# Performance work log

Measured on AMD Instinct MI355X. Metric: run time of the kernel, lower is better.

Reference implementation:

```python
import jax, jax.numpy as jnp
import numpy as np

N, E, L, H, C, F_IN = 50000, 800000, 3, 8, 16, 128  # nodes, edges, layers, heads, per-head dim, input dim
NEG_SLOPE = 0.2


def setup_inputs() -> dict:
    key = jax.random.key(0)
    k = jax.random.split(key, 8)
    scale = 0.1
    x = jax.random.normal(k[0], (N, F_IN), dtype=jnp.float32)
    Ws = jax.random.normal(k[1], (L, F_IN, H * C), dtype=jnp.float32) * scale
    att_src = jax.random.normal(k[2], (L, H, C), dtype=jnp.float32) * scale
    att_dst = jax.random.normal(k[3], (L, H, C), dtype=jnp.float32) * scale
    biases = jnp.zeros((L, H * C), dtype=jnp.float32)
    fc_w = jax.random.normal(k[4], (H * C, C), dtype=jnp.float32) * scale
    fc_b = jnp.zeros((C,), dtype=jnp.float32)
    edge_index = jax.random.randint(k[5], (2, E), 0, N, dtype=jnp.int64)
    return {"x": x, "Ws": Ws, "att_src": att_src, "att_dst": att_dst,
            "biases": biases, "fc_w": fc_w, "fc_b": fc_b, "edge_index": edge_index}


def _gat_layer(x, W, a_src, a_dst, b, src, dst):
    # x: [N, F]; W: [F, H*C]; a_src/a_dst: [H, C]; src/dst: [E+N] (self-loops included)
    n = x.shape[0]
    h = (x @ W).reshape(n, H, C)                      # [N, H, C]
    e_src = jnp.einsum('nhc,hc->nh', h, a_src)        # [N, H]
    e_dst = jnp.einsum('nhc,hc->nh', h, a_dst)
    e = jax.nn.leaky_relu(e_src[src] + e_dst[dst], NEG_SLOPE)   # [E+N, H]
    # segment softmax over incoming edges of each target node
    emax = jax.ops.segment_max(e, dst, num_segments=n)          # [N, H]
    ex = jnp.exp(e - emax[dst])
    denom = jax.ops.segment_sum(ex, dst, num_segments=n)        # [N, H]
    alpha = ex / (denom[dst] + 1e-16)                            # [E+N, H]
    out = jax.ops.segment_sum(alpha[:, :, None] * h[src], dst, num_segments=n)  # [N, H, C]
    return out.reshape(n, H * C) + b


def reference(x, Ws, att_src, att_dst, biases, fc_w, fc_b, edge_index):
    loop = jnp.arange(N, dtype=edge_index.dtype)
    src = jnp.concatenate([edge_index[0], loop])  # add self-loops (PyG default)
    dst = jnp.concatenate([edge_index[1], loop])
    h = x
    for l in range(L):
        h = _gat_layer(h, Ws[l], att_src[l], att_dst[l], biases[l], src, dst)
        h = jax.nn.elu(h)
    return h @ fc_w + fc_b  # [N, C]
```

## Files before the change

kernel.cpp:

```cpp
#include <hip/hip_runtime.h>
#include <hip/hip_bf16.h>


#define GAT_F 128
#define GAT_H 8
#define GAT_C 16

__device__ __forceinline__ float bf2f(unsigned short u) {
    union { unsigned int i; float f; } x; x.i = ((unsigned int)u) << 16; return x.f;
}
__device__ __forceinline__ float bfhi2f(unsigned int u) {
    union { unsigned int i; float f; } x; x.i = u & 0xFFFF0000u; return x.f;
}
__device__ __forceinline__ float bflo2f(unsigned int u) {
    union { unsigned int i; float f; } x; x.i = u << 16; return x.f;
}
__device__ __forceinline__ unsigned int pk_bf16(float a, float b) {
    union { float f; unsigned int i; } ua, ub;
    ua.f = a; ub.f = b;
    unsigned int ra = (ua.i + 0x7FFFu + ((ua.i >> 16) & 1u)) >> 16;
    unsigned int rb = (ub.i + 0x7FFFu + ((ub.i >> 16) & 1u)) & 0xFFFF0000u;
    return ra | rb;
}
__device__ __forceinline__ float ldf(const void* p, size_t i, int isf32) {
    return isf32 ? ((const float*)p)[i] : bf2f(((const unsigned short*)p)[i]);
}
__device__ __forceinline__ int ldei(const int* ei, int i, int is64) {
    return is64 ? ei[2 * (size_t)i] : ei[i];
}

__global__ void k_detect(const unsigned short* __restrict__ xb,
                         const int* __restrict__ ei, int* flags) {
    __shared__ int nan_cnt, zero_cnt;
    if (threadIdx.x == 0) { nan_cnt = 0; zero_cnt = 0; }
    __syncthreads();
    int t = threadIdx.x;
    int ln = 0;
    for (int i = t; i < 8192; i += 256) {
        unsigned short u = xb[i];
        if ((u & 0x7F80) == 0x7F80) ln++;
    }
    int lz = 0;
    for (int i = t; i < 2048; i += 256) {
        if (ei[2 * i + 1] == 0) lz++;
    }
    if (ln) atomicAdd(&nan_cnt, ln);
    if (lz) atomicAdd(&zero_cnt, lz);
    __syncthreads();
    if (t == 0) {
        flags[0] = (nan_cnt > 3) ? 1 : 0;
        flags[1] = (zero_cnt > 1024) ? 1 : 0;
    }
}

__global__ void k_init_deg(int* deg, int n) {
    int i = blockIdx.x * 256 + threadIdx.x;
    if (i < n) deg[i] = 1;
}

__global__ void k_count_deg(const int* __restrict__ ei, int* deg, int E,
                            const int* __restrict__ flags) {
    int k = blockIdx.x * 256 + threadIdx.x;
    int is64 = flags[1];
    if (k < E) atomicAdd(&deg[ldei(ei, E + k, is64)], 1);
}

__global__ __launch_bounds__(256) void k_scan_blk(
    const int* __restrict__ deg, int* __restrict__ rp_local,
    int* __restrict__ bsum, int n)
{
    int b = blockIdx.x, t = threadIdx.x;
    int i0 = b * 1024 + t * 4;
    int v0 = 0, v1 = 0, v2 = 0, v3 = 0;
    if (i0 + 3 < n) {
        int4 d = *(const int4*)(deg + i0);
        v0 = d.x; v1 = d.y; v2 = d.z; v3 = d.w;
    } else {
        if (i0     < n) v0 = deg[i0];
        if (i0 + 1 < n) v1 = deg[i0 + 1];
        if (i0 + 2 < n) v2 = deg[i0 + 2];
        if (i0 + 3 < n) v3 = deg[i0 + 3];
    }
    int s = v0 + v1 + v2 + v3;
    int lane = t & 63, wid = t >> 6;
    int sc = s;
    #pragma unroll
    for (int off = 1; off < 64; off <<= 1) {
        int o = __shfl_up(sc, off);
        if (lane >= off) sc += o;
    }
    __shared__ int wsum[4];
    if (lane == 63) wsum[wid] = sc;
    __syncthreads();
    int woff = 0;
    #pragma unroll
    for (int w2 = 0; w2 < 4; w2++) if (w2 < wid) woff += wsum[w2];
    int excl = woff + sc - s;
    if (i0     < n) rp_local[i0]     = excl;
    if (i0 + 1 < n) rp_local[i0 + 1] = excl + v0;
    if (i0 + 2 < n) rp_local[i0 + 2] = excl + v0 + v1;
    if (i0 + 3 < n) rp_local[i0 + 3] = excl + v0 + v1 + v2;
    if (t == 255) bsum[b] = woff + sc;
}

__global__ __launch_bounds__(256) void k_scan_top(
    int* __restrict__ bsum, int* __restrict__ rowptr, int nb, int n)
{
    __shared__ int sh[1024];
    int t = threadIdx.x;
    for (int i = t; i < 1024; i += 256) sh[i] = (i < nb) ? bsum[i] : 0;
    __syncthreads();
    for (int off = 1; off < 1024; off <<= 1) {
        int vals[4];
        #pragma unroll
        for (int k = 0; k < 4; k++) {
            int i = t + 256 * k;
            vals[k] = (i >= off) ? sh[i - off] : 0;
        }
        __syncthreads();
        #pragma unroll
        for (int k = 0; k < 4; k++) sh[t + 256 * k] += vals[k];
        __syncthreads();
    }
    for (int i = t; i < nb; i += 256) bsum[i] = (i == 0) ? 0 : sh[i - 1];
    if (t == 0) rowptr[n] = sh[nb - 1];
}

__global__ void k_place_add(int* __restrict__ rowptr, const int* __restrict__ bsum,
                            int* __restrict__ adj, int* __restrict__ cursor, int n)
{
    int i = blockIdx.x * 256 + threadIdx.x;
    if (i < n) {
        int r = rowptr[i] + bsum[i >> 10];
        rowptr[i] = r;
        adj[r] = i;
        cursor[i] = 1;
    }
    if (blockIdx.x == 0 && threadIdx.x < 8) adj[rowptr[n] + threadIdx.x] = 0;
}

__global__ void k_scatter(const int* __restrict__ ei, const int* __restrict__ rowptr,
                          int* __restrict__ cursor, int* __restrict__ adj, int E,
                          const int* __restrict__ flags) {
    int k = blockIdx.x * 256 + threadIdx.x;
    int is64 = flags[1];
    if (k < E) {
        int s = ldei(ei, k, is64);
        int d = ldei(ei, E + k, is64);
        int p = atomicAdd(&cursor[d], 1);
        adj[rowptr[d] + p] = s;
    }
}

__global__ __launch_bounds__(256) void k_gemm_scores(
    const void* __restrict__ xin, int x_is_input,
    const void* __restrict__ W, long w_off,
    const void* __restrict__ asrc, const void* __restrict__ adst, long a_off,
    unsigned int* __restrict__ hout, float* __restrict__ es, float* __restrict__ ed,
    int n, const int* __restrict__ flags)
{
    __shared__ float xs[32 * 132];
    int isf32 = flags[0];
    int t = threadIdx.x;
    int row0 = blockIdx.x * 32;

    if (!x_is_input) {
        const float4* xg = (const float4*)xin;
        for (int i = t; i < 32 * GAT_F / 4; i += 256) {
            int r = i >> 5, k4 = i & 31;
            int gr = row0 + r;
            float4 v = make_float4(0.f, 0.f, 0.f, 0.f);
            if (gr < n) v = xg[gr * 32 + k4];
            *(float4*)&xs[r * 132 + k4 * 4] = v;
        }
    } else {
        for (int i = t; i < 32 * GAT_F; i += 256) {
            int r = i >> 7, k = i & 127;
            int gr = row0 + r;
            float v = 0.f;
            if (gr < n) v = ldf(xin, (size_t)gr * GAT_F + k, isf32);
            xs[r * 132 + k] = v;
        }
    }
    __syncthreads();

    int tx = t & 31, ty = t >> 5;
    int r0 = ty * 4, c0 = tx * 4;
    float acc[4][4];
    #pragma unroll
    for (int i = 0; i < 4; i++)
        #pragma unroll
        for (int j = 0; j < 4; j++) acc[i][j] = 0.f;

    if (isf32) {
        const float4* Wg = (const float4*)((const float*)W + w_off);
        for (int k = 0; k < GAT_F; k++) {
            float4 wv = Wg[k * 32 + tx];
            #pragma unroll
            for (int i = 0; i < 4; i++) {
                float xv = xs[(r0 + i) * 132 + k];
                acc[i][0] += xv * wv.x; acc[i][1] += xv * wv.y;
                acc[i][2] += xv * wv.z; acc[i][3] += xv * wv.w;
            }
        }
    } else {
        const ushort4* Wg = (const ushort4*)((const unsigned short*)W + w_off);
        for (int k = 0; k < GAT_F; k++) {
            ushort4 u4 = Wg[k * 32 + tx];
            float4 wv = make_float4(bf2f(u4.x), bf2f(u4.y), bf2f(u4.z), bf2f(u4.w));
            #pragma unroll
            for (int i = 0; i < 4; i++) {
                float xv = xs[(r0 + i) * 132 + k];
                acc[i][0] += xv * wv.x; acc[i][1] += xv * wv.y;
                acc[i][2] += xv * wv.z; acc[i][3] += xv * wv.w;
            }
        }
    }

    int head = tx >> 2;
    int cb = (tx & 3) * 4;
    float av[4], dv[4];
    #pragma unroll
    for (int j = 0; j < 4; j++) {
        av[j] = ldf(asrc, a_off + head * GAT_C + cb + j, isf32);
        dv[j] = ldf(adst, a_off + head * GAT_C + cb + j, isf32);
    }
    #pragma unroll
    for (int i = 0; i < 4; i++) {
        float ps = acc[i][0] * av[0] + acc[i][1] * av[1] + acc[i][2] * av[2] + acc[i][3] * av[3];
        float pd = acc[i][0] * dv[0] + acc[i][1] * dv[1] + acc[i][2] * dv[2] + acc[i][3] * dv[3];
        ps += __shfl_xor(ps, 1); ps += __shfl_xor(ps, 2);
        pd += __shfl_xor(pd, 1); pd += __shfl_xor(pd, 2);
        int gr = row0 + r0 + i;
        if ((tx & 3) == 0 && gr < n) {
            es[(size_t)gr * GAT_H + head] = ps;
            ed[(size_t)gr * GAT_H + head] = pd;
        }
        if (gr < n) {
            uint2 packed = make_uint2(pk_bf16(acc[i][0], acc[i][1]),
                                      pk_bf16(acc[i][2], acc[i][3]));
            *(uint2*)(hout + gr * 64 + (c0 >> 1)) = packed;
        }
    }
}

__global__ __launch_bounds__(256) void k_aggregate(
    const unsigned int* __restrict__ hb,
    const float* __restrict__ es, const float* __restrict__ ed,
    const int* __restrict__ rowptr, const int* __restrict__ adj,
    const void* __restrict__ bias, long b_off, float* __restrict__ out, int n,
    const int* __restrict__ flags)
{
    int isf32 = flags[0];
    int lane = threadIdx.x & 63;
    int node = blockIdx.x * 4 + (threadIdx.x >> 6);
    if (node >= n) return;
    int base = rowptr[node];
    int deg = rowptr[node + 1] - base;
    int head = lane >> 3;
    float edv = ed[node * 8 + head];

    float acc0 = 0.f, acc1 = 0.f, lsum = 0.f;
    for (int j0 = 0; j0 < deg; j0 += 4) {
        int sa = adj[base + j0];
        int sb = adj[base + j0 + 1];
        int sc = adj[base + j0 + 2];
        int sd = adj[base + j0 + 3];
        float va = es[sa * 8 + head] + edv;
        float vb = es[sb * 8 + head] + edv;
        float vc = es[sc * 8 + head] + edv;
        float vd = es[sd * 8 + head] + edv;
        unsigned int ha = hb[sa * 64 + lane];
        unsigned int hbv = hb[sb * 64 + lane];
        unsigned int hc = hb[sc * 64 + lane];
        unsigned int hd = hb[sd * 64 + lane];
        va = va > 0.f ? va : 0.2f * va;
        vb = vb > 0.f ? vb : 0.2f * vb;
        vc = vc > 0.f ? vc : 0.2f * vc;
        vd = vd > 0.f ? vd : 0.2f * vd;
        float pa = __expf(va);
        float pb = (j0 + 1 < deg) ? __expf(vb) : 0.f;
        float pc = (j0 + 2 < deg) ? __expf(vc) : 0.f;
        float pd = (j0 + 3 < deg) ? __expf(vd) : 0.f;
        lsum += (pa + pb) + (pc + pd);
        acc0 += pa * bflo2f(ha) + pb * bflo2f(hbv) + pc * bflo2f(hc) + pd * bflo2f(hd);
        acc1 += pa * bfhi2f(ha) + pb * bfhi2f(hbv) + pc * bfhi2f(hc) + pd * bfhi2f(hd);
    }

    float inv = 1.f / (lsum + 1e-16f);
    int ch = lane << 1;
    float o0 = acc0 * inv + ldf(bias, b_off + ch, isf32);
    float o1 = acc1 * inv + ldf(bias, b_off + ch + 1, isf32);
    o0 = o0 > 0.f ? o0 : (__expf(o0) - 1.f);
    o1 = o1 > 0.f ? o1 : (__expf(o1) - 1.f);
    *(float2*)(out + (size_t)node * GAT_F + ch) = make_float2(o0, o1);
}

__global__ __launch_bounds__(256) void k_fc(
    const float* __restrict__ h, const void* __restrict__ fw,
    const void* __restrict__ fb, void* __restrict__ out, int n,
    const int* __restrict__ flags)
{
    __shared__ float fws[GAT_F * GAT_C];
    int isf32 = flags[0];
    int t = threadIdx.x;
    for (int i = t; i < GAT_F * GAT_C; i += 256)
        fws[i] = ldf(fw, i, isf32);
    __syncthreads();
    int row = blockIdx.x * 256 + t;
    if (row >= n) return;
    float acc[16];
    #pragma unroll
    for (int c = 0; c < 16; c++) acc[c] = ldf(fb, c, isf32);
    const float4* hr = (const float4*)(h + (size_t)row * GAT_F);
    for (int k4 = 0; k4 < GAT_F / 4; k4++) {
        float4 xv = hr[k4];
        float xs4[4] = {xv.x, xv.y, xv.z, xv.w};
        #pragma unroll
        for (int kk = 0; kk < 4; kk++) {
            int k = k4 * 4 + kk;
            const float4* wr = (const float4*)(fws + k * GAT_C);
            #pragma unroll
            for (int c4 = 0; c4 < 4; c4++) {
                float4 wv = wr[c4];
                acc[c4 * 4 + 0] += xs4[kk] * wv.x;
                acc[c4 * 4 + 1] += xs4[kk] * wv.y;
                acc[c4 * 4 + 2] += xs4[kk] * wv.z;
                acc[c4 * 4 + 3] += xs4[kk] * wv.w;
            }
        }
    }
    if (isf32) {
        float* o = (float*)out + (size_t)row * GAT_C;
        #pragma unroll
        for (int c = 0; c < 16; c++) o[c] = acc[c];
    } else {
        __hip_bfloat16* o = (__hip_bfloat16*)out + (size_t)row * GAT_C;
        #pragma unroll
        for (int c = 0; c < 16; c++) o[c] = __float2bfloat16(acc[c]);
    }
}

extern "C" void kernel_launch(void* const* d_in, const int* in_sizes, int n_in,
                              void* d_out, int out_size, void* d_ws, size_t ws_size,
                              hipStream_t stream) {
    const void* x      = d_in[0];
    const void* Ws     = d_in[1];
    const void* att_s  = d_in[2];
    const void* att_d  = d_in[3];
    const void* biases = d_in[4];
    const void* fc_w   = d_in[5];
    const void* fc_b   = d_in[6];
    const int*  ei     = (const int*)d_in[7];

    const int N  = in_sizes[0] / GAT_F;
    const int E  = in_sizes[7] / 2;
    const int L  = in_sizes[1] / (GAT_F * GAT_F);
    const int ET = E + N;

    char* w = (char*)d_ws;
    int* flags        = (int*)w;          w += 64;
    float* hA         = (float*)w;        w += (size_t)N * GAT_F * 4;
    unsigned int* hB  = (unsigned int*)w; w += (size_t)N * 64 * 4;
    float* es         = (float*)w;        w += (size_t)N * GAT_H * 4;
    float* ed         = (float*)w;        w += (size_t)N * GAT_H * 4;
    int* rowptr       = (int*)w;          w += (((size_t)(N + 1) * 4 + 15) & ~15ull);
    int* cursor       = (int*)w;          w += (size_t)N * 4;
    int* bsum         = (int*)w;          w += 1024 * 4;
    int* adj          = (int*)w;          w += (size_t)(ET + 16) * 4;

    int nb_n = (N + 255) / 256;
    int nb_e = (E + 255) / 256;
    int nb_s = (N + 1023) / 1024;

    k_detect<<<1, 256, 0, stream>>>((const unsigned short*)x, ei, flags);

    k_init_deg<<<nb_n, 256, 0, stream>>>(cursor, N);
    k_count_deg<<<nb_e, 256, 0, stream>>>(ei, cursor, E, flags);
    k_scan_blk<<<nb_s, 256, 0, stream>>>(cursor, rowptr, bsum, N);
    k_scan_top<<<1, 256, 0, stream>>>(bsum, rowptr, nb_s, N);
    k_place_add<<<nb_n, 256, 0, stream>>>(rowptr, bsum, adj, cursor, N);
    k_scatter<<<nb_e, 256, 0, stream>>>(ei, rowptr, cursor, adj, E, flags);

    int nb_g = (N + 31) / 32;
    int nb_a = (N + 3) / 4;
    for (int l = 0; l < L; l++) {
        k_gemm_scores<<<nb_g, 256, 0, stream>>>(
            (l == 0) ? x : (const void*)hA, (l == 0) ? 1 : 0,
            Ws, (long)l * GAT_F * GAT_F,
            att_s, att_d, (long)l * GAT_H * GAT_C,
            hB, es, ed, N, flags);
        k_aggregate<<<nb_a, 256, 0, stream>>>(
            hB, es, ed, rowptr, adj,
            biases, (long)l * GAT_F, hA, N, flags);
    }
    k_fc<<<nb_n, 256, 0, stream>>>(hA, fc_w, fc_b, d_out, N, flags);
}
```

Before: 459.3 us.

## Use bf16 MFMA for layer GEMM and fold attention vectors into weights

Replaces the fp32 FMA tiled GEMM with a bf16 MFMA kernel over 64-row tiles. A prep kernel transposes the weights to bf16 and precomputes W·a_src and W·a_dst as 16 extra output columns, so the attention scores come straight out of the MFMA instead of needing shuffle reductions. This cuts GEMM compute time but adds a prep launch and rounds the inputs and score weights to bf16, which may change accuracy. It also loads the full 144x128 weight tile into shared memory in every block.

```diff
diff --git a/kernel.cpp b/kernel.cpp
--- a/kernel.cpp
+++ b/kernel.cpp
@@ -5,6 +5,9 @@
 #define GAT_F 128
 #define GAT_H 8
 #define GAT_C 16
+
+typedef __attribute__((ext_vector_type(8))) short bf16x8;
+typedef __attribute__((ext_vector_type(4))) float f32x4;
 
 __device__ __forceinline__ float bf2f(unsigned short u) {
     union { unsigned int i; float f; } x; x.i = ((unsigned int)u) << 16; return x.f;
@@ -22,6 +25,10 @@
     unsigned int rb = (ub.i + 0x7FFFu + ((ub.i >> 16) & 1u)) & 0xFFFF0000u;
     return ra | rb;
 }
+__device__ __forceinline__ unsigned short f2bf(float a) {
+    union { float f; unsigned int i; } ua; ua.f = a;
+    return (unsigned short)((ua.i + 0x7FFFu + ((ua.i >> 16) & 1u)) >> 16);
+}
 __device__ __forceinline__ float ldf(const void* p, size_t i, int isf32) {
     return isf32 ? ((const float*)p)[i] : bf2f(((const unsigned short*)p)[i]);
 }
@@ -50,6 +57,35 @@
     if (t == 0) {
         flags[0] = (nan_cnt > 3) ? 1 : 0;
         flags[1] = (zero_cnt > 1024) ? 1 : 0;
+    }
+}
+
+__global__ void k_prep(const void* __restrict__ W, const void* __restrict__ asrc,
+                       const void* __restrict__ adst,
+                       unsigned short* __restrict__ wt, unsigned short* __restrict__ wa,
+                       int Lw, const int* __restrict__ flags) {
+    int isf32 = flags[0];
+    int b = blockIdx.x, t = threadIdx.x;
+    if (b < Lw * 64) {
+        int gid = b * 256 + t;
+        int l = gid >> 14, r = gid & 16383;
+        int c = r >> 7, k = r & 127;
+        float v = ldf(W, (size_t)l * 16384 + k * 128 + c, isf32);
+        wt[gid] = f2bf(v);
+    } else {
+        int id = (b - Lw * 64) * 256 + t;
+        int l = id >> 11, q = id & 2047;
+        int j = q >> 7, k = q & 127;
+        int head = j & 7;
+        const void* av = (j < 8) ? asrc : adst;
+        float acc = 0.f;
+        #pragma unroll
+        for (int cc = 0; cc < 16; cc++) {
+            float w = ldf(W, (size_t)l * 16384 + k * 128 + head * 16 + cc, isf32);
+            float a = ldf(av, (size_t)l * 128 + head * 16 + cc, isf32);
+            acc += w * a;
+        }
+        wa[id] = f2bf(acc);
     }
 }
 
@@ -152,94 +188,89 @@
     }
 }
 
-__global__ __launch_bounds__(256) void k_gemm_scores(
+__global__ __launch_bounds__(256) void k_gemm_mfma(
     const void* __restrict__ xin, int x_is_input,
-    const void* __restrict__ W, long w_off,
-    const void* __restrict__ asrc, const void* __restrict__ adst, long a_off,
-    unsigned int* __restrict__ hout, float* __restrict__ es, float* __restrict__ ed,
+    const unsigned short* __restrict__ wt,
+    const unsigned short* __restrict__ wa,
+    unsigned int* __restrict__ hb, float* __restrict__ es, float* __restrict__ ed,
     int n, const int* __restrict__ flags)
 {
-    __shared__ float xs[32 * 132];
+    __shared__ unsigned short xl[64 * 136];
+    __shared__ unsigned short wl[144 * 136];
     int isf32 = flags[0];
     int t = threadIdx.x;
-    int row0 = blockIdx.x * 32;
-
-    if (!x_is_input) {
+    int row0 = blockIdx.x * 64;
+
+    if (isf32 || !x_is_input) {
         const float4* xg = (const float4*)xin;
-        for (int i = t; i < 32 * GAT_F / 4; i += 256) {
-            int r = i >> 5, k4 = i & 31;
+        for (int i = t; i < 2048; i += 256) {
+            int r = i >> 5, c4 = i & 31;
             int gr = row0 + r;
-            float4 v = make_float4(0.f, 0.f, 0.f, 0.f);
-            if (gr < n) v = xg[gr * 32 + k4];
-            *(float4*)&xs[r * 132 + k4 * 4] = v;
+            uint2 u = make_uint2(0u, 0u);
+            if (gr < n) {
+                float4 v = xg[(size_t)gr * 32 + c4];
+                u = make_uint2(pk_bf16(v.x, v.y), pk_bf16(v.z, v.w));
+            }
+            *(uint2*)&xl[r * 136 + c4 * 4] = u;
         }
     } else {
-        for (int i = t; i < 32 * GAT_F; i += 256) {
-            int r = i >> 7, k = i & 127;
+        const ushort4* xg = (const ushort4*)xin;
+        for (int i = t; i < 2048; i += 256) {
+            int r = i >> 5, c4 = i & 31;
             int gr = row0 + r;
-            float v = 0.f;
-            if (gr < n) v = ldf(xin, (size_t)gr * GAT_F + k, isf32);
-            xs[r * 132 + k] = v;
-        }
-    }
-    __syncthreads();
-
-    int tx = t & 31, ty = t >> 5;
-    int r0 = ty * 4, c0 = tx * 4;
-    float acc[4][4];
-    #pragma unroll
-    for (int i = 0; i < 4; i++)
-        #pragma unroll
-        for (int j = 0; j < 4; j++) acc[i][j] = 0.f;
-
-    if (isf32) {
-        const float4* Wg = (const float4*)((const float*)W + w_off);
-        for (int k = 0; k < GAT_F; k++) {
-            float4 wv = Wg[k * 32 + tx];
-            #pragma unroll
-            for (int i = 0; i < 4; i++) {
-                float xv = xs[(r0 + i) * 132 + k];
-                acc[i][0] += xv * wv.x; acc[i][1] += xv * wv.y;
-                acc[i][2] += xv * wv.z; acc[i][3] += xv * wv.w;
-            }
-        }
-    } else {
-        const ushort4* Wg = (const ushort4*)((const unsigned short*)W + w_off);
-        for (int k = 0; k < GAT_F; k++) {
-            ushort4 u4 = Wg[k * 32 + tx];
-            float4 wv = make_float4(bf2f(u4.x), bf2f(u4.y), bf2f(u4.z), bf2f(u4.w));
-            #pragma unroll
-            for (int i = 0; i < 4; i++) {
-                float xv = xs[(r0 + i) * 132 + k];
-                acc[i][0] += xv * wv.x; acc[i][1] += xv * wv.y;
-                acc[i][2] += xv * wv.z; acc[i][3] += xv * wv.w;
-            }
-        }
-    }
-
-    int head = tx >> 2;
-    int cb = (tx & 3) * 4;
-    float av[4], dv[4];
-    #pragma unroll
-    for (int j = 0; j < 4; j++) {
-        av[j] = ldf(asrc, a_off + head * GAT_C + cb + j, isf32);
-        dv[j] = ldf(adst, a_off + head * GAT_C + cb + j, isf32);
-    }
-    #pragma unroll
-    for (int i = 0; i < 4; i++) {
-        float ps = acc[i][0] * av[0] + acc[i][1] * av[1] + acc[i][2] * av[2] + acc[i][3] * av[3];
-        float pd = acc[i][0] * dv[0] + acc[i][1] * dv[1] + acc[i][2] * dv[2] + acc[i][3] * dv[3];
-        ps += __shfl_xor(ps, 1); ps += __shfl_xor(ps, 2);
-        pd += __shfl_xor(pd, 1); pd += __shfl_xor(pd, 2);
-        int gr = row0 + r0 + i;
-        if ((tx & 3) == 0 && gr < n) {
-            es[(size_t)gr * GAT_H + head] = ps;
-            ed[(size_t)gr * GAT_H + head] = pd;
-        }
-        if (gr < n) {
-            uint2 packed = make_uint2(pk_bf16(acc[i][0], acc[i][1]),
-                                      pk_bf16(acc[i][2], acc[i][3]));
-            *(uint2*)(hout + gr * 64 + (c0 >> 1)) = packed;
+            ushort4 v = make_ushort4(0, 0, 0, 0);
+            if (gr < n) v = xg[(size_t)gr * 32 + c4];
+            *(ushort4*)&xl[r * 136 + c4 * 4] = v;
+        }
+    }
+    {
+        const ushort4* wg = (const ushort4*)wt;
+        for (int i = t; i < 4096; i += 256) {
+            int c = i >> 5, k4 = i & 31;
+            *(ushort4*)&wl[c * 136 + k4 * 4] = wg[i];
+        }
+        const ushort4* wag = (const ushort4*)wa;
+        for (int i = t; i < 512; i += 256) {
+            int j = i >> 5, k4 = i & 31;
+            *(ushort4*)&wl[(128 + j) * 136 + k4 * 4] = wag[i];
+        }
+    }
+    __syncthreads();
+
+    int lane = t & 63, wid = t >> 6, quad = lane >> 4, col = lane & 15;
+    f32x4 acc[9];
+    #pragma unroll
+    for (int ct = 0; ct < 9; ct++) acc[ct] = (f32x4){0.f, 0.f, 0.f, 0.f};
+
+    #pragma unroll
+    for (int ks = 0; ks < 4; ks++) {
+        int k0 = ks * 32;
+        bf16x8 af = *(const bf16x8*)&xl[(wid * 16 + col) * 136 + k0 + quad * 8];
+        #pragma unroll
+        for (int ct = 0; ct < 9; ct++) {
+            bf16x8 bf = *(const bf16x8*)&wl[(ct * 16 + col) * 136 + k0 + quad * 8];
+            acc[ct] = __builtin_amdgcn_mfma_f32_16x16x32_bf16(af, bf, acc[ct], 0, 0, 0);
+        }
+    }
+
+    #pragma unroll
+    for (int ct = 0; ct < 8; ct++) {
+        #pragma unroll
+        for (int r = 0; r < 4; r++) {
+            int grow = row0 + wid * 16 + quad * 4 + r;
+            float v = acc[ct][r];
+            float vp = __shfl_xor(v, 1);
+            if (!(lane & 1) && grow < n)
+                hb[(size_t)grow * 64 + ct * 8 + (col >> 1)] = pk_bf16(v, vp);
+        }
+    }
+    #pragma unroll
+    for (int r = 0; r < 4; r++) {
+        int grow = row0 + wid * 16 + quad * 4 + r;
+        float v = acc[8][r];
+        if (grow < n) {
+            if (col < 8) es[(size_t)grow * 8 + col] = v;
+            else         ed[(size_t)grow * 8 + col - 8] = v;
         }
     }
 }
@@ -359,21 +390,24 @@
     const int ET = E + N;
 
     char* w = (char*)d_ws;
-    int* flags        = (int*)w;          w += 64;
-    float* hA         = (float*)w;        w += (size_t)N * GAT_F * 4;
-    unsigned int* hB  = (unsigned int*)w; w += (size_t)N * 64 * 4;
-    float* es         = (float*)w;        w += (size_t)N * GAT_H * 4;
-    float* ed         = (float*)w;        w += (size_t)N * GAT_H * 4;
-    int* rowptr       = (int*)w;          w += (((size_t)(N + 1) * 4 + 15) & ~15ull);
-    int* cursor       = (int*)w;          w += (size_t)N * 4;
-    int* bsum         = (int*)w;          w += 1024 * 4;
-    int* adj          = (int*)w;          w += (size_t)(ET + 16) * 4;
+    int* flags         = (int*)w;            w += 64;
+    float* hA          = (float*)w;          w += (size_t)N * GAT_F * 4;
+    unsigned int* hB   = (unsigned int*)w;   w += (size_t)N * 64 * 4;
+    float* es          = (float*)w;          w += (size_t)N * GAT_H * 4;
+    float* ed          = (float*)w;          w += (size_t)N * GAT_H * 4;
+    int* rowptr        = (int*)w;            w += (((size_t)(N + 1) * 4 + 15) & ~15ull);
+    int* cursor        = (int*)w;            w += (size_t)N * 4;
+    int* bsum          = (int*)w;            w += 1024 * 4;
+    int* adj           = (int*)w;            w += (size_t)(ET + 16) * 4;
+    unsigned short* wt = (unsigned short*)w; w += (size_t)L * 16384 * 2;
+    unsigned short* wa = (unsigned short*)w; w += (size_t)L * 2048 * 2;
 
     int nb_n = (N + 255) / 256;
     int nb_e = (E + 255) / 256;
     int nb_s = (N + 1023) / 1024;
 
     k_detect<<<1, 256, 0, stream>>>((const unsigned short*)x, ei, flags);
+    k_prep<<<L * 64 + L * 8, 256, 0, stream>>>(Ws, att_s, att_d, wt, wa, L, flags);
 
     k_init_deg<<<nb_n, 256, 0, stream>>>(cursor, N);
     k_count_deg<<<nb_e, 256, 0, stream>>>(ei, cursor, E, flags);
@@ -382,13 +416,12 @@
     k_place_add<<<nb_n, 256, 0, stream>>>(rowptr, bsum, adj, cursor, N);
     k_scatter<<<nb_e, 256, 0, stream>>>(ei, rowptr, cursor, adj, E, flags);
 
-    int nb_g = (N + 31) / 32;
+    int nb_g = (N + 63) / 64;
     int nb_a = (N + 3) / 4;
     for (int l = 0; l < L; l++) {
-        k_gemm_scores<<<nb_g, 256, 0, stream>>>(
+        k_gemm_mfma<<<nb_g, 256, 0, stream>>>(
             (l == 0) ? x : (const void*)hA, (l == 0) ? 1 : 0,
-            Ws, (long)l * GAT_F * GAT_F,
-            att_s, att_d, (long)l * GAT_H * GAT_C,
+            wt + (size_t)l * 16384, wa + (size_t)l * 2048,
             hB, es, ed, N, flags);
         k_aggregate<<<nb_a, 256, 0, stream>>>(
             hB, es, ed, rowptr, adj,
```

New measurement: 409.0 us. 1.12x faster.
